# Performance work log

Hardware: AMD Instinct MI355X
Metric: run time of the kernel (lower is better)

The kernel has to match this reference:

```python
import jax, jax.numpy as jnp
import numpy as np

NUM_HEADS = 16
EMB_DIM = 1024
HEAD_DIM = EMB_DIM // NUM_HEADS


def setup_inputs() -> dict:
    key = jax.random.key(0)
    k1, k2, k3, k4 = jax.random.split(key, 4)
    B, S = 2, 2048
    X = jax.random.normal(k1, (B, S, EMB_DIM), dtype=jnp.float32)
    # torch Linear(in, out, bias=False): y = x @ W.T ; store as [in, out]
    Wq = jax.random.normal(k2, (EMB_DIM, EMB_DIM), dtype=jnp.float32) * (EMB_DIM ** -0.5)
    Wk = jax.random.normal(k3, (EMB_DIM, HEAD_DIM), dtype=jnp.float32) * (EMB_DIM ** -0.5)
    Wv = jax.random.normal(k4, (EMB_DIM, HEAD_DIM), dtype=jnp.float32) * (EMB_DIM ** -0.5)
    return {"X": X, "Wq": Wq, "Wk": Wk, "Wv": Wv}


def reference(X, Wq, Wk, Wv):
    B, S, E = X.shape
    H, D = NUM_HEADS, HEAD_DIM
    q = (X @ Wq).reshape(B, S, H, D).transpose(0, 2, 1, 3)  # [B,H,S,D]
    k = X @ Wk  # [B,S,D] shared K head
    v = X @ Wv  # [B,S,D] shared V head
    scores = jnp.einsum('bhsd,btd->bhst', q, k) / jnp.sqrt(jnp.float32(D))
    causal = jnp.tril(jnp.ones((S, S), dtype=bool))
    scores = jnp.where(causal, scores, -jnp.inf)
    probs = jax.nn.softmax(scores, axis=-1)  # [B,H,S,S]
    out = jnp.einsum('bhst,btd->bhsd', probs, v)  # [B,H,S,D]
    return out.transpose(0, 2, 1, 3).reshape(B, S, E)
```

## Files before the change

### kernel.cpp

```cpp
#include <hip/hip_runtime.h>
#include <stdint.h>

#define NH   16
#define EMB  1024
#define HD   64
#define BSZ  2
#define SEQ  2048
#define NROW (BSZ * SEQ)

typedef __attribute__((ext_vector_type(8))) short bf16x8;
typedef __attribute__((ext_vector_type(4))) float f32x4;

#define CQ 0.18033688011112042f

__device__ __forceinline__ uint16_t f2bf(float f) {
    union { float f; uint32_t i; } v; v.f = f;
    uint32_t r = v.i + 0x7FFFu + ((v.i >> 16) & 1u);
    return (uint16_t)(r >> 16);
}
__device__ __forceinline__ uint32_t pack2(float a, float b) {
    return (uint32_t)f2bf(a) | ((uint32_t)f2bf(b) << 16);
}
__device__ __forceinline__ uint32_t cvtpk(float a, float b) {
    uint32_t r;
    asm("v_cvt_pk_bf16_f32 %0, %1, %2" : "=v"(r) : "v"(a), "v"(b));
    return r;
}

__device__ __forceinline__ void gl2lds16(const uint16_t* g, uint16_t* l) {
    __builtin_amdgcn_global_load_lds(
        static_cast<const uint32_t*>(static_cast<const void*>(g)),
        static_cast<uint32_t*>(static_cast<void*>(l)), 16, 0, 0);
}

__global__ __launch_bounds__(256) void prep(
    const float* __restrict__ X, uint16_t* __restrict__ Xbf,
    const float* __restrict__ Wq, const float* __restrict__ Wk,
    const float* __restrict__ Wv, uint16_t* __restrict__ Wqt,
    uint16_t* __restrict__ Wkt, uint16_t* __restrict__ Wvt)
{
    __shared__ uint16_t T[64][72];
    const int tid = threadIdx.x;
    if (blockIdx.x < 2048) {
        size_t idx = ((size_t)blockIdx.x * 256 + tid) * 8;
        float4 a = *(const float4*)&X[idx];
        float4 b = *(const float4*)&X[idx + 4];
        *(uint4*)&Xbf[idx] = make_uint4(pack2(a.x, a.y), pack2(a.z, a.w),
                                        pack2(b.x, b.y), pack2(b.z, b.w));
        return;
    }
    const int id = blockIdx.x - 2048;
    const float* W; uint16_t* Wt; int k0, n0, ldw;
    if (id < 256)      { W = Wq; Wt = Wqt; k0 = (id >> 4) * 64; n0 = (id & 15) * 64; ldw = EMB; }
    else if (id < 272) { W = Wk; Wt = Wkt; k0 = (id - 256) * 64; n0 = 0; ldw = HD; }
    else               { W = Wv; Wt = Wvt; k0 = (id - 272) * 64; n0 = 0; ldw = HD; }
    const float scl = (id < 256) ? CQ : 1.0f;

    const int r = tid >> 2, c4 = (tid & 3) * 16;
#pragma unroll
    for (int i = 0; i < 4; ++i) {
        float4 wv = *(const float4*)&W[(size_t)(k0 + r) * ldw + n0 + c4 + 4 * i];
        T[r][c4 + 4 * i + 0] = f2bf(wv.x * scl); T[r][c4 + 4 * i + 1] = f2bf(wv.y * scl);
        T[r][c4 + 4 * i + 2] = f2bf(wv.z * scl); T[r][c4 + 4 * i + 3] = f2bf(wv.w * scl);
    }
    __syncthreads();
    const int n = tid >> 2, kk = (tid & 3) * 16;
    uint32_t o[8];
#pragma unroll
    for (int i = 0; i < 8; ++i)
        o[i] = (uint32_t)T[kk + 2 * i][n] | ((uint32_t)T[kk + 2 * i + 1][n] << 16);
    uint16_t* dst = &Wt[(size_t)(n0 + n) * EMB + k0 + kk];
    *(uint4*)dst       = make_uint4(o[0], o[1], o[2], o[3]);
    *(uint4*)(dst + 8) = make_uint4(o[4], o[5], o[6], o[7]);
}

__global__ __launch_bounds__(256) void qkv_gemm_mfma5(
    const uint16_t* __restrict__ Xbf, const uint16_t* __restrict__ Wqt,
    const uint16_t* __restrict__ Wkt, const uint16_t* __restrict__ Wvt,
    uint16_t* __restrict__ Qbf, uint16_t* __restrict__ Kbf,
    uint16_t* __restrict__ Vtbf)
{
    const int tid  = threadIdx.x;
    const int w    = tid >> 6, lane = tid & 63;
    const int l    = lane & 15, quad = lane >> 4;
    const int wm   = w & 1, wn = w >> 1;

    const int lin  = blockIdx.x + 9 * blockIdx.y;
    const int lin2 = (lin & 7) * 72 + (lin >> 3);
    const int nt   = lin2 % 9;
    const int m0   = (lin2 / 9) * 64;

    __shared__ uint16_t As[2][64 * 64];
    __shared__ uint16_t Bs[2][128 * 64];

    const uint16_t* gA[2]; uint32_t ldsA[2];
    const uint16_t* gB[4]; uint32_t ldsB[4];
#pragma unroll
    for (int i = 0; i < 2; ++i) {
        int G = (w * 2 + i) * 64 + lane;
        int r = G >> 3, cg = (G & 7) ^ (r & 7);
        gA[i] = &Xbf[(size_t)(m0 + r) * EMB + cg * 8];
        ldsA[i] = (w * 2 + i) * 512;
    }
#pragma unroll
    for (int i = 0; i < 4; ++i) {
        int G = (w * 4 + i) * 64 + lane;
        int r = G >> 3, cg = (G & 7) ^ (r & 7);
        const uint16_t* bs;
        if (nt < 8)      bs = &Wqt[(size_t)(nt * 128 + r) * EMB + cg * 8];
        else if (r < 64) bs = &Wkt[(size_t)r * EMB + cg * 8];
        else             bs = &Wvt[(size_t)(r - 64) * EMB + cg * 8];
        gB[i] = bs;
        ldsB[i] = (w * 4 + i) * 512;
    }

    uint32_t offA[2][2], offB[4][2];
#pragma unroll
    for (int i = 0; i < 2; ++i)
#pragma unroll
        for (int kh = 0; kh < 2; ++kh) {
            int row = 32 * wm + 16 * i + l;
            offA[i][kh] = row * 64 + (((kh * 4 + quad) ^ (row & 7)) * 8);
        }
#pragma unroll
    for (int j = 0; j < 4; ++j)
#pragma unroll
        for (int kh = 0; kh < 2; ++kh) {
            int row = 64 * wn + 16 * j + l;
            offB[j][kh] = row * 64 + (((kh * 4 + quad) ^ (row & 7)) * 8);
        }

    f32x4 acc[2][4] = {};

#pragma unroll
    for (int i = 0; i < 2; ++i) { gl2lds16(gA[i], &As[0][ldsA[i]]); gA[i] += 64; }
#pragma unroll
    for (int i = 0; i < 4; ++i) { gl2lds16(gB[i], &Bs[0][ldsB[i]]); gB[i] += 64; }
    __syncthreads();

    for (int ks = 0; ks < 16; ++ks) {
        const int cur = ks & 1, nxt = cur ^ 1;
        if (ks < 15) {
#pragma unroll
            for (int i = 0; i < 2; ++i) { gl2lds16(gA[i], &As[nxt][ldsA[i]]); gA[i] += 64; }
#pragma unroll
            for (int i = 0; i < 4; ++i) { gl2lds16(gB[i], &Bs[nxt][ldsB[i]]); gB[i] += 64; }
        }
#pragma unroll
        for (int kh = 0; kh < 2; ++kh) {
            bf16x8 af[2], bfr[4];
#pragma unroll
            for (int i = 0; i < 2; ++i) af[i] = *(const bf16x8*)&As[cur][offA[i][kh]];
#pragma unroll
            for (int j = 0; j < 4; ++j) bfr[j] = *(const bf16x8*)&Bs[cur][offB[j][kh]];
#pragma unroll
            for (int i = 0; i < 2; ++i)
#pragma unroll
                for (int j = 0; j < 4; ++j)
                    acc[i][j] = __builtin_amdgcn_mfma_f32_16x16x32_bf16(
                        af[i], bfr[j], acc[i][j], 0, 0, 0);
        }
        __syncthreads();
    }

    if (nt < 8) {
#pragma unroll
        for (int i = 0; i < 2; ++i)
#pragma unroll
            for (int j = 0; j < 4; ++j)
#pragma unroll
                for (int r = 0; r < 4; ++r)
                    Qbf[(size_t)(m0 + 32 * wm + 16 * i + 4 * quad + r) * EMB
                        + nt * 128 + 64 * wn + 16 * j + l] = f2bf(acc[i][j][r]);
    } else if (wn == 0) {
#pragma unroll
        for (int i = 0; i < 2; ++i)
#pragma unroll
            for (int j = 0; j < 4; ++j)
#pragma unroll
                for (int r = 0; r < 4; ++r)
                    Kbf[(size_t)(m0 + 32 * wm + 16 * i + 4 * quad + r) * HD
                        + 16 * j + l] = f2bf(acc[i][j][r]);
    } else {
#pragma unroll
        for (int i = 0; i < 2; ++i)
#pragma unroll
            for (int j = 0; j < 4; ++j)
#pragma unroll
                for (int r = 0; r < 4; ++r)
                    Vtbf[(size_t)(16 * j + l) * NROW
                         + m0 + 32 * wm + 16 * i + 4 * quad + r] = f2bf(acc[i][j][r]);
    }
}

__global__ __launch_bounds__(256) void mqa_attn(
    const uint16_t* __restrict__ Qbf, const uint16_t* __restrict__ Kbf,
    const uint16_t* __restrict__ Vtbf, float* __restrict__ Out)
{
    const int tid  = threadIdx.x;
    const int w    = tid >> 6;
    const int lane = tid & 63;
    const int l    = lane & 15;
    const int quad = lane >> 4;
    const int i  = blockIdx.x;
    const int h  = blockIdx.y, b = blockIdx.z;
    const int qt0 = 31 - i, qt1 = i;
    const int q00 = qt0 * 64, q01 = qt1 * 64;

    __shared__ __align__(16) uint16_t Ks[2][4096];
    __shared__ __align__(16) uint16_t Vs[2][4096];
    __shared__ __align__(16) uint16_t Ps[2][4096];

    const uint16_t* kSrc[2]; const uint16_t* vSrc[2]; uint32_t dstE[2];
#pragma unroll
    for (int i2 = 0; i2 < 2; ++i2) {
        int G = (w * 2 + i2) * 64 + lane;
        int r = G >> 3, g = G & 7;
        int pr = (r & 32) + ((r >> 2) & 3) * 8 + ((r & 16) >> 2) + (r & 3);
        int cg = g ^ (r & 7);
        kSrc[i2] = &Kbf[(size_t)(b * SEQ + pr) * HD + cg * 8];
        vSrc[i2] = &Vtbf[(size_t)r * NROW + b * SEQ + cg * 8];
        dstE[i2] = (uint32_t)(w * 2 + i2) * 512;
    }

#pragma unroll
    for (int i2 = 0; i2 < 2; ++i2) {
        gl2lds16(kSrc[i2], &Ks[0][dstE[i2]]);
        gl2lds16(vSrc[i2], &Vs[0][dstE[i2]]);
        kSrc[i2] += 64 * HD;
        vSrc[i2] += 64;
    }
#pragma unroll
    for (int t = 0; t < 2; ++t) {
        const int q0t = t ? q01 : q00;
#pragma unroll
        for (int i2 = 0; i2 < 2; ++i2) {
            int G = (w * 2 + i2) * 64 + lane;
            int r = G >> 3, g = G & 7;
            int cg = g ^ (r & 7);
            gl2lds16(&Qbf[(size_t)(b * SEQ + q0t + r) * EMB + h * HD + cg * 8],
                     &Ps[t][dstE[i2]]);
        }
    }
    __syncthreads();

    bf16x8 qf[2][2];
    {
        const int row = 16 * w + l;
#pragma unroll
        for (int t = 0; t < 2; ++t) {
            qf[t][0] = *(const bf16x8*)&Ps[t][row * 64 + (((0 + quad) ^ (row & 7)) * 8)];
            qf[t][1] = *(const bf16x8*)&Ps[t][row * 64 + (((4 + quad) ^ (row & 7)) * 8)];
        }
    }

    uint32_t off[4][2];
#pragma unroll
    for (int ts = 0; ts < 4; ++ts)
#pragma unroll
        for (int kh = 0; kh < 2; ++kh)
            off[ts][kh] = (16 * ts + l) * 64 + (((4 * kh + quad) ^ (l & 7)) * 8);

    bf16x8 ones;
#pragma unroll
    for (int j = 0; j < 8; ++j) ones[j] = (short)0x3F80;

    f32x4 accO[2][4] = {};
    f32x4 accSum[2] = {};
    const int qi_l = 16 * w + l;

    auto body = [&](int kb, bool DO1, bool M0, bool M1) __attribute__((always_inline)) {
        const int cur = kb & 1, nxt = cur ^ 1;

        bf16x8 ka[4][2], vb[4][2];
#pragma unroll
        for (int ts = 0; ts < 4; ++ts) {
            ka[ts][0] = *(const bf16x8*)&Ks[cur][off[ts][0]];
            ka[ts][1] = *(const bf16x8*)&Ks[cur][off[ts][1]];
            vb[ts][0] = *(const bf16x8*)&Vs[cur][off[ts][0]];
            vb[ts][1] = *(const bf16x8*)&Vs[cur][off[ts][1]];
        }

        if (kb < qt0) {
#pragma unroll
            for (int i2 = 0; i2 < 2; ++i2) {
                gl2lds16(kSrc[i2], &Ks[nxt][dstE[i2]]);
                gl2lds16(vSrc[i2], &Vs[nxt][dstE[i2]]);
                kSrc[i2] += 64 * HD;
                vSrc[i2] += 64;
            }
        }

        f32x4 accS0[4] = {}, accS1[4] = {};
#pragma unroll
        for (int ts = 0; ts < 4; ++ts) {
            accS0[ts] = __builtin_amdgcn_mfma_f32_16x16x32_bf16(ka[ts][0], qf[0][0], accS0[ts], 0, 0, 0);
            accS0[ts] = __builtin_amdgcn_mfma_f32_16x16x32_bf16(ka[ts][1], qf[0][1], accS0[ts], 0, 0, 0);
        }
        if (DO1) {
#pragma unroll
            for (int ts = 0; ts < 4; ++ts) {
                accS1[ts] = __builtin_amdgcn_mfma_f32_16x16x32_bf16(ka[ts][0], qf[1][0], accS1[ts], 0, 0, 0);
                accS1[ts] = __builtin_amdgcn_mfma_f32_16x16x32_bf16(ka[ts][1], qf[1][1], accS1[ts], 0, 0, 0);
            }
        }

        {
            float pv[16];
#pragma unroll
            for (int ts = 0; ts < 4; ++ts)
#pragma unroll
                for (int r = 0; r < 4; ++r)
                    pv[4 * ts + r] = exp2f(accS0[ts][r]);
            if (M0) {
#pragma unroll
                for (int ts = 0; ts < 4; ++ts)
#pragma unroll
                    for (int r = 0; r < 4; ++r)
                        if ((((ts & 2) << 4) + ((ts & 1) << 2) + 8 * quad + r) > qi_l)
                            pv[4 * ts + r] = 0.f;
            }
            union { uint32_t u[4]; bf16x8 v; } A0, A1;
#pragma unroll
            for (int j = 0; j < 4; ++j) A0.u[j] = cvtpk(pv[2 * j],     pv[2 * j + 1]);
#pragma unroll
            for (int j = 0; j < 4; ++j) A1.u[j] = cvtpk(pv[8 + 2 * j], pv[9 + 2 * j]);
#pragma unroll
            for (int tn = 0; tn < 4; ++tn) {
                accO[0][tn] = __builtin_amdgcn_mfma_f32_16x16x32_bf16(A0.v, vb[tn][0], accO[0][tn], 0, 0, 0);
                accO[0][tn] = __builtin_amdgcn_mfma_f32_16x16x32_bf16(A1.v, vb[tn][1], accO[0][tn], 0, 0, 0);
            }
            accSum[0] = __builtin_amdgcn_mfma_f32_16x16x32_bf16(A0.v, ones, accSum[0], 0, 0, 0);
            accSum[0] = __builtin_amdgcn_mfma_f32_16x16x32_bf16(A1.v, ones, accSum[0], 0, 0, 0);
        }
        if (DO1) {
            float pv[16];
#pragma unroll
            for (int ts = 0; ts < 4; ++ts)
#pragma unroll
                for (int r = 0; r < 4; ++r)
                    pv[4 * ts + r] = exp2f(accS1[ts][r]);
            if (M1) {
#pragma unroll
                for (int ts = 0; ts < 4; ++ts)
#pragma unroll
                    for (int r = 0; r < 4; ++r)
                        if ((((ts & 2) << 4) + ((ts & 1) << 2) + 8 * quad + r) > qi_l)
                            pv[4 * ts + r] = 0.f;
            }
            union { uint32_t u[4]; bf16x8 v; } A0, A1;
#pragma unroll
            for (int j = 0; j < 4; ++j) A0.u[j] = cvtpk(pv[2 * j],     pv[2 * j + 1]);
#pragma unroll
            for (int j = 0; j < 4; ++j) A1.u[j] = cvtpk(pv[8 + 2 * j], pv[9 + 2 * j]);
#pragma unroll
            for (int tn = 0; tn < 4; ++tn) {
                accO[1][tn] = __builtin_amdgcn_mfma_f32_16x16x32_bf16(A0.v, vb[tn][0], accO[1][tn], 0, 0, 0);
                accO[1][tn] = __builtin_amdgcn_mfma_f32_16x16x32_bf16(A1.v, vb[tn][1], accO[1][tn], 0, 0, 0);
            }
            accSum[1] = __builtin_amdgcn_mfma_f32_16x16x32_bf16(A0.v, ones, accSum[1], 0, 0, 0);
            accSum[1] = __builtin_amdgcn_mfma_f32_16x16x32_bf16(A1.v, ones, accSum[1], 0, 0, 0);
        }

        if (kb < qt0) __syncthreads();
    };

    for (int kb = 0; kb < qt1; ++kb) body(kb, true,  false, false);
    body(qt1, true,  false, true);
    for (int kb = qt1 + 1; kb < qt0; ++kb) body(kb, false, false, false);
    body(qt0, false, true,  false);

#pragma unroll
    for (int t = 0; t < 2; ++t) {
        const int q0t = t ? q01 : q00;
#pragma unroll
        for (int r = 0; r < 4; ++r) {
            float invr = 1.0f / accSum[t][r];
            const int row = q0t + 16 * w + 4 * quad + r;
#pragma unroll
            for (int tn = 0; tn < 4; ++tn)
                Out[(size_t)(b * SEQ + row) * EMB + h * HD + 16 * tn + l] =
                    accO[t][tn][r] * invr;
        }
    }
}

__global__ __launch_bounds__(256) void qkv_gemm_vec(
    const float* __restrict__ X,  const float* __restrict__ Wq,
    const float* __restrict__ Wk, const float* __restrict__ Wv,
    uint16_t* __restrict__ Qbf, uint16_t* __restrict__ Kbf,
    uint16_t* __restrict__ Vtbf)
{
    const int tid = threadIdx.x;
    const int tx = tid & 15, ty = tid >> 4;
    const int bx = blockIdx.x;
    const int m0 = blockIdx.y * 64;

    const float* W; int ldw, n0;
    if (bx < 16)       { W = Wq; ldw = EMB; n0 = bx * 64; }
    else if (bx == 16) { W = Wk; ldw = HD;  n0 = 0; }
    else               { W = Wv; ldw = HD;  n0 = 0; }

    __shared__ float sA[64][17];
    __shared__ float sB[16][64];

    float acc[4][4] = {};
    const int arow = tid >> 2, acol = (tid & 3) * 4;
    const int brow = tid >> 4, bcol = (tid & 15) * 4;

    for (int k0 = 0; k0 < EMB; k0 += 16) {
        float4 fa = *(const float4*)&X[(size_t)(m0 + arow) * EMB + k0 + acol];
        float4 fb = *(const float4*)&W[(size_t)(k0 + brow) * ldw + n0 + bcol];
        sA[arow][acol + 0] = fa.x; sA[arow][acol + 1] = fa.y;
        sA[arow][acol + 2] = fa.z; sA[arow][acol + 3] = fa.w;
        sB[brow][bcol + 0] = fb.x; sB[brow][bcol + 1] = fb.y;
        sB[brow][bcol + 2] = fb.z; sB[brow][bcol + 3] = fb.w;
        __syncthreads();
#pragma unroll
        for (int kk = 0; kk < 16; ++kk) {
            float a0 = sA[4 * ty + 0][kk];
            float a1 = sA[4 * ty + 1][kk];
            float a2 = sA[4 * ty + 2][kk];
            float a3 = sA[4 * ty + 3][kk];
            float4 bq = *(const float4*)&sB[kk][4 * tx];
            acc[0][0] += a0 * bq.x; acc[0][1] += a0 * bq.y; acc[0][2] += a0 * bq.z; acc[0][3] += a0 * bq.w;
            acc[1][0] += a1 * bq.x; acc[1][1] += a1 * bq.y; acc[1][2] += a1 * bq.z; acc[1][3] += a1 * bq.w;
            acc[2][0] += a2 * bq.x; acc[2][1] += a2 * bq.y; acc[2][2] += a2 * bq.z; acc[2][3] += a2 * bq.w;
            acc[3][0] += a3 * bq.x; acc[3][1] += a3 * bq.y; acc[3][2] += a3 * bq.z; acc[3][3] += a3 * bq.w;
        }
        __syncthreads();
    }

    if (bx < 16) {
#pragma unroll
        for (int i = 0; i < 4; ++i) {
            ushort4 u; u.x = f2bf(acc[i][0] * CQ); u.y = f2bf(acc[i][1] * CQ);
            u.z = f2bf(acc[i][2] * CQ); u.w = f2bf(acc[i][3] * CQ);
            *(ushort4*)&Qbf[(size_t)(m0 + 4 * ty + i) * EMB + n0 + 4 * tx] = u;
        }
    } else if (bx == 16) {
#pragma unroll
        for (int i = 0; i < 4; ++i) {
            ushort4 u; u.x = f2bf(acc[i][0]); u.y = f2bf(acc[i][1]);
            u.z = f2bf(acc[i][2]); u.w = f2bf(acc[i][3]);
            *(ushort4*)&Kbf[(size_t)(m0 + 4 * ty + i) * HD + 4 * tx] = u;
        }
    } else {
#pragma unroll
        for (int j = 0; j < 4; ++j) {
            ushort4 u; u.x = f2bf(acc[0][j]); u.y = f2bf(acc[1][j]);
            u.z = f2bf(acc[2][j]); u.w = f2bf(acc[3][j]);
            *(ushort4*)&Vtbf[(size_t)(4 * tx + j) * NROW + m0 + 4 * ty] = u;
        }
    }
}

extern "C" void kernel_launch(void* const* d_in, const int* in_sizes, int n_in,
                              void* d_out, int out_size, void* d_ws, size_t ws_size,
                              hipStream_t stream) {
    const float* X  = (const float*)d_in[0];
    const float* Wq = (const float*)d_in[1];
    const float* Wk = (const float*)d_in[2];
    const float* Wv = (const float*)d_in[3];
    float* OutP = (float*)d_out;

    char* ws = (char*)d_ws;
    const size_t MB = 1024 * 1024;
    const size_t KB = 1024;
    uint16_t* Xbf  = (uint16_t*)(ws);
    uint16_t* Qbf  = (uint16_t*)(ws + 8 * MB);
    uint16_t* Wqt  = (uint16_t*)(ws + 16 * MB);
    uint16_t* Wkt  = (uint16_t*)(ws + 18 * MB);
    uint16_t* Wvt  = (uint16_t*)(ws + 18 * MB + 256 * KB);
    uint16_t* Kbf  = (uint16_t*)(ws + 18 * MB + 512 * KB);
    uint16_t* Vtbf = (uint16_t*)(ws + 19 * MB);

    if (ws_size >= 20 * MB) {
        prep<<<2336, 256, 0, stream>>>(X, Xbf, Wq, Wk, Wv, Wqt, Wkt, Wvt);
        qkv_gemm_mfma5<<<dim3(9, 64), 256, 0, stream>>>(Xbf, Wqt, Wkt, Wvt,
                                                        Qbf, Kbf, Vtbf);
        mqa_attn<<<dim3(16, NH, BSZ), 256, 0, stream>>>(Qbf, Kbf, Vtbf, OutP);
    } else {
        uint16_t* QbfS  = (uint16_t*)ws;
        uint16_t* KbfS  = (uint16_t*)(ws + 8 * MB);
        uint16_t* VtbfS = (uint16_t*)(ws + 8 * MB + 512 * KB);
        qkv_gemm_vec<<<dim3(18, 64), 256, 0, stream>>>(X, Wq, Wk, Wv, QbfS, KbfS, VtbfS);
        mqa_attn<<<dim3(16, NH, BSZ), 256, 0, stream>>>(QbfS, KbfS, VtbfS, OutP);
    }
}
```

Before: 128.8 us.

## Split attention warps across query and key halves with LDS cross-warp reduction

```diff
diff --git a/kernel.cpp b/kernel.cpp
--- a/kernel.cpp
+++ b/kernel.cpp
@@ -202,6 +202,8 @@
     const int lane = tid & 63;
     const int l    = lane & 15;
     const int quad = lane >> 4;
+    const int wq   = w & 1;
+    const int wk   = w >> 1;
     const int i  = blockIdx.x;
     const int h  = blockIdx.y, b = blockIdx.z;
     const int qt0 = 31 - i, qt1 = i;
@@ -210,6 +212,8 @@
     __shared__ __align__(16) uint16_t Ks[2][4096];
     __shared__ __align__(16) uint16_t Vs[2][4096];
     __shared__ __align__(16) uint16_t Ps[2][4096];
+    __shared__ __align__(16) float    XB[16][64][4];
+    __shared__ __align__(16) float    SB[4][64][4];
 
     const uint16_t* kSrc[2]; const uint16_t* vSrc[2]; uint32_t dstE[2];
 #pragma unroll
@@ -244,42 +248,49 @@
     }
     __syncthreads();
 
-    bf16x8 qf[2][2];
-    {
-        const int row = 16 * w + l;
-#pragma unroll
-        for (int t = 0; t < 2; ++t) {
-            qf[t][0] = *(const bf16x8*)&Ps[t][row * 64 + (((0 + quad) ^ (row & 7)) * 8)];
-            qf[t][1] = *(const bf16x8*)&Ps[t][row * 64 + (((4 + quad) ^ (row & 7)) * 8)];
-        }
-    }
-
-    uint32_t off[4][2];
-#pragma unroll
-    for (int ts = 0; ts < 4; ++ts)
-#pragma unroll
-        for (int kh = 0; kh < 2; ++kh)
-            off[ts][kh] = (16 * ts + l) * 64 + (((4 * kh + quad) ^ (l & 7)) * 8);
+    bf16x8 qf[2][2][2];
+#pragma unroll
+    for (int t = 0; t < 2; ++t)
+#pragma unroll
+        for (int qs = 0; qs < 2; ++qs) {
+            const int row = 32 * wq + 16 * qs + l;
+            qf[t][qs][0] = *(const bf16x8*)&Ps[t][row * 64 + (((0 + quad) ^ (row & 7)) * 8)];
+            qf[t][qs][1] = *(const bf16x8*)&Ps[t][row * 64 + (((4 + quad) ^ (row & 7)) * 8)];
+        }
+
+    uint32_t offK[2][2], offV[4];
+#pragma unroll
+    for (int ts = 0; ts < 2; ++ts)
+#pragma unroll
+        for (int kh = 0; kh < 2; ++kh) {
+            int row = 32 * wk + 16 * ts + l;
+            offK[ts][kh] = row * 64 + (((kh * 4 + quad) ^ (row & 7)) * 8);
+        }
+#pragma unroll
+    for (int tn = 0; tn < 4; ++tn) {
+        int row = 16 * tn + l;
+        offV[tn] = row * 64 + (((4 * wk + quad) ^ (row & 7)) * 8);
+    }
 
     bf16x8 ones;
 #pragma unroll
     for (int j = 0; j < 8; ++j) ones[j] = (short)0x3F80;
 
-    f32x4 accO[2][4] = {};
-    f32x4 accSum[2] = {};
-    const int qi_l = 16 * w + l;
+    f32x4 accO[2][2][4] = {};
+    f32x4 accSum[2][2] = {};
 
     auto body = [&](int kb, bool DO1, bool M0, bool M1) __attribute__((always_inline)) {
         const int cur = kb & 1, nxt = cur ^ 1;
 
-        bf16x8 ka[4][2], vb[4][2];
-#pragma unroll
-        for (int ts = 0; ts < 4; ++ts) {
-            ka[ts][0] = *(const bf16x8*)&Ks[cur][off[ts][0]];
-            ka[ts][1] = *(const bf16x8*)&Ks[cur][off[ts][1]];
-            vb[ts][0] = *(const bf16x8*)&Vs[cur][off[ts][0]];
-            vb[ts][1] = *(const bf16x8*)&Vs[cur][off[ts][1]];
-        }
+        bf16x8 ka[2][2], vb[4];
+#pragma unroll
+        for (int ts = 0; ts < 2; ++ts) {
+            ka[ts][0] = *(const bf16x8*)&Ks[cur][offK[ts][0]];
+            ka[ts][1] = *(const bf16x8*)&Ks[cur][offK[ts][1]];
+        }
+#pragma unroll
+        for (int tn = 0; tn < 4; ++tn)
+            vb[tn] = *(const bf16x8*)&Vs[cur][offV[tn]];
 
         if (kb < qt0) {
 #pragma unroll
@@ -291,75 +302,48 @@
             }
         }
 
-        f32x4 accS0[4] = {}, accS1[4] = {};
-#pragma unroll
-        for (int ts = 0; ts < 4; ++ts) {
-            accS0[ts] = __builtin_amdgcn_mfma_f32_16x16x32_bf16(ka[ts][0], qf[0][0], accS0[ts], 0, 0, 0);
-            accS0[ts] = __builtin_amdgcn_mfma_f32_16x16x32_bf16(ka[ts][1], qf[0][1], accS0[ts], 0, 0, 0);
-        }
-        if (DO1) {
-#pragma unroll
-            for (int ts = 0; ts < 4; ++ts) {
-                accS1[ts] = __builtin_amdgcn_mfma_f32_16x16x32_bf16(ka[ts][0], qf[1][0], accS1[ts], 0, 0, 0);
-                accS1[ts] = __builtin_amdgcn_mfma_f32_16x16x32_bf16(ka[ts][1], qf[1][1], accS1[ts], 0, 0, 0);
+#pragma unroll
+        for (int t = 0; t < 2; ++t) {
+            if (t == 1 && !DO1) break;
+            const bool M = t ? M1 : M0;
+            f32x4 accS[2][2] = {};
+#pragma unroll
+            for (int qs = 0; qs < 2; ++qs)
+#pragma unroll
+                for (int ts = 0; ts < 2; ++ts) {
+                    accS[qs][ts] = __builtin_amdgcn_mfma_f32_16x16x32_bf16(
+                        ka[ts][0], qf[t][qs][0], accS[qs][ts], 0, 0, 0);
+                    accS[qs][ts] = __builtin_amdgcn_mfma_f32_16x16x32_bf16(
+                        ka[ts][1], qf[t][qs][1], accS[qs][ts], 0, 0, 0);
+                }
+#pragma unroll
+            for (int qs = 0; qs < 2; ++qs) {
+                float pvq[8];
+#pragma unroll
+                for (int ts = 0; ts < 2; ++ts)
+#pragma unroll
+                    for (int r = 0; r < 4; ++r)
+                        pvq[4 * ts + r] = exp2f(accS[qs][ts][r]);
+                if (M) {
+#pragma unroll
+                    for (int ts = 0; ts < 2; ++ts)
+#pragma unroll
+                        for (int r = 0; r < 4; ++r)
+                            if ((32 * wk + 8 * quad + 4 * ts + r) >
+                                (32 * wq + 16 * qs + l))
+                                pvq[4 * ts + r] = 0.f;
+                }
+                union { uint32_t u[4]; bf16x8 v; } A;
+#pragma unroll
+                for (int j = 0; j < 4; ++j)
+                    A.u[j] = cvtpk(pvq[2 * j], pvq[2 * j + 1]);
+#pragma unroll
+                for (int tn = 0; tn < 4; ++tn)
+                    accO[t][qs][tn] = __builtin_amdgcn_mfma_f32_16x16x32_bf16(
+                        A.v, vb[tn], accO[t][qs][tn], 0, 0, 0);
+                accSum[t][qs] = __builtin_amdgcn_mfma_f32_16x16x32_bf16(
+                    A.v, ones, accSum[t][qs], 0, 0, 0);
             }
-        }
-
-        {
-            float pv[16];
-#pragma unroll
-            for (int ts = 0; ts < 4; ++ts)
-#pragma unroll
-                for (int r = 0; r < 4; ++r)
-                    pv[4 * ts + r] = exp2f(accS0[ts][r]);
-            if (M0) {
-#pragma unroll
-                for (int ts = 0; ts < 4; ++ts)
-#pragma unroll
-                    for (int r = 0; r < 4; ++r)
-                        if ((((ts & 2) << 4) + ((ts & 1) << 2) + 8 * quad + r) > qi_l)
-                            pv[4 * ts + r] = 0.f;
-            }
-            union { uint32_t u[4]; bf16x8 v; } A0, A1;
-#pragma unroll
-            for (int j = 0; j < 4; ++j) A0.u[j] = cvtpk(pv[2 * j],     pv[2 * j + 1]);
-#pragma unroll
-            for (int j = 0; j < 4; ++j) A1.u[j] = cvtpk(pv[8 + 2 * j], pv[9 + 2 * j]);
-#pragma unroll
-            for (int tn = 0; tn < 4; ++tn) {
-                accO[0][tn] = __builtin_amdgcn_mfma_f32_16x16x32_bf16(A0.v, vb[tn][0], accO[0][tn], 0, 0, 0);
-                accO[0][tn] = __builtin_amdgcn_mfma_f32_16x16x32_bf16(A1.v, vb[tn][1], accO[0][tn], 0, 0, 0);
-            }
-            accSum[0] = __builtin_amdgcn_mfma_f32_16x16x32_bf16(A0.v, ones, accSum[0], 0, 0, 0);
-            accSum[0] = __builtin_amdgcn_mfma_f32_16x16x32_bf16(A1.v, ones, accSum[0], 0, 0, 0);
-        }
-        if (DO1) {
-            float pv[16];
-#pragma unroll
-            for (int ts = 0; ts < 4; ++ts)
-#pragma unroll
-                for (int r = 0; r < 4; ++r)
-                    pv[4 * ts + r] = exp2f(accS1[ts][r]);
-            if (M1) {
-#pragma unroll
-                for (int ts = 0; ts < 4; ++ts)
-#pragma unroll
-                    for (int r = 0; r < 4; ++r)
-                        if ((((ts & 2) << 4) + ((ts & 1) << 2) + 8 * quad + r) > qi_l)
-                            pv[4 * ts + r] = 0.f;
-            }
-            union { uint32_t u[4]; bf16x8 v; } A0, A1;
-#pragma unroll
-            for (int j = 0; j < 4; ++j) A0.u[j] = cvtpk(pv[2 * j],     pv[2 * j + 1]);
-#pragma unroll
-            for (int j = 0; j < 4; ++j) A1.u[j] = cvtpk(pv[8 + 2 * j], pv[9 + 2 * j]);
-#pragma unroll
-            for (int tn = 0; tn < 4; ++tn) {
-                accO[1][tn] = __builtin_amdgcn_mfma_f32_16x16x32_bf16(A0.v, vb[tn][0], accO[1][tn], 0, 0, 0);
-                accO[1][tn] = __builtin_amdgcn_mfma_f32_16x16x32_bf16(A1.v, vb[tn][1], accO[1][tn], 0, 0, 0);
-            }
-            accSum[1] = __builtin_amdgcn_mfma_f32_16x16x32_bf16(A0.v, ones, accSum[1], 0, 0, 0);
-            accSum[1] = __builtin_amdgcn_mfma_f32_16x16x32_bf16(A1.v, ones, accSum[1], 0, 0, 0);
         }
 
         if (kb < qt0) __syncthreads();
@@ -370,17 +354,66 @@
     for (int kb = qt1 + 1; kb < qt0; ++kb) body(kb, false, false, false);
     body(qt0, false, true,  false);
 
-#pragma unroll
-    for (int t = 0; t < 2; ++t) {
-        const int q0t = t ? q01 : q00;
-#pragma unroll
-        for (int r = 0; r < 4; ++r) {
-            float invr = 1.0f / accSum[t][r];
-            const int row = q0t + 16 * w + 4 * quad + r;
+    __syncthreads();
+
+    if (wk == 1) {
+#pragma unroll
+        for (int qs = 0; qs < 2; ++qs) {
 #pragma unroll
             for (int tn = 0; tn < 4; ++tn)
-                Out[(size_t)(b * SEQ + row) * EMB + h * HD + 16 * tn + l] =
-                    accO[t][tn][r] * invr;
+                *(f32x4*)&XB[(wq * 2 + qs) * 4 + tn][lane][0] = accO[0][qs][tn];
+            *(f32x4*)&SB[wq * 2 + qs][lane][0] = accSum[0][qs];
+        }
+    }
+    __syncthreads();
+    if (wk == 0) {
+#pragma unroll
+        for (int qs = 0; qs < 2; ++qs) {
+            f32x4 stot = accSum[0][qs];
+            stot += *(const f32x4*)&SB[wq * 2 + qs][lane][0];
+#pragma unroll
+            for (int r = 0; r < 4; ++r) {
+                float inv = 1.0f / stot[r];
+                const int row = q00 + 32 * wq + 16 * qs + 4 * quad + r;
+#pragma unroll
+                for (int tn = 0; tn < 4; ++tn) {
+                    float o = accO[0][qs][tn][r] +
+                              XB[(wq * 2 + qs) * 4 + tn][lane][r];
+                    Out[(size_t)(b * SEQ + row) * EMB + h * HD + 16 * tn + l] =
+                        o * inv;
+                }
+            }
+        }
+    }
+    __syncthreads();
+
+    if (wk == 0) {
+#pragma unroll
+        for (int qs = 0; qs < 2; ++qs) {
+#pragma unroll
+            for (int tn = 0; tn < 4; ++tn)
+                *(f32x4*)&XB[(wq * 2 + qs) * 4 + tn][lane][0] = accO[1][qs][tn];
+            *(f32x4*)&SB[wq * 2 + qs][lane][0] = accSum[1][qs];
+        }
+    }
+    __syncthreads();
+    if (wk == 1) {
+#pragma unroll
+        for (int qs = 0; qs < 2; ++qs) {
+            f32x4 stot = accSum[1][qs];
+            stot += *(const f32x4*)&SB[wq * 2 + qs][lane][0];
+#pragma unroll
+            for (int r = 0; r < 4; ++r) {
+                float inv = 1.0f / stot[r];
+                const int row = q01 + 32 * wq + 16 * qs + 4 * quad + r;
+#pragma unroll
+                for (int tn = 0; tn < 4; ++tn) {
+                    float o = accO[1][qs][tn][r] +
+                              XB[(wq * 2 + qs) * 4 + tn][lane][r];
+                    Out[(size_t)(b * SEQ + row) * EMB + h * HD + 16 * tn + l] =
+                        o * inv;
+                }
+            }
         }
     }
 }
```

After: 127.0 us. About the same (-1.4%).
